# Kernel optimization log

Measured on AMD Instinct MI355X. Metric: run time of the kernel, lower is better.

## Reference

```python
import jax, jax.numpy as jnp
import numpy as np


def _ln(x, w, b):
    m = x.mean(-1, keepdims=True)
    v = x.var(-1, keepdims=True)
    return (x - m) * jax.lax.rsqrt(v + 1e-5) * w + b


def setup_inputs() -> dict:
    key = jax.random.key(0)
    ks = jax.random.split(key, 12)
    B, Cm, T, D, H = 8, 192, 2048, 512, 1536
    n_fft, hop = 1024, 256
    nF = n_fft // 2 + 1
    s = 0.05
    rn = lambda k, shape: jax.random.normal(k, shape, jnp.float32) * s
    window = (0.5 - 0.5 * jnp.cos(2.0 * jnp.pi * jnp.arange(n_fft, dtype=jnp.float32) / n_fft))
    return dict(
        mel=jax.random.normal(ks[0], (B, Cm, T), jnp.float32),
        embed_w=rn(ks[1], (D, Cm, 7)), embed_b=rn(ks[2], (D,)),
        norm_w=jnp.ones((D,), jnp.float32), norm_b=jnp.zeros((D,), jnp.float32),
        blk_dw_w=rn(ks[3], (8, D, 1, 7)), blk_dw_b=rn(ks[4], (8, D)),
        blk_norm_w=jnp.ones((8, D), jnp.float32), blk_norm_b=jnp.zeros((8, D), jnp.float32),
        blk_pw1_w=rn(ks[5], (8, H, D)), blk_pw1_b=rn(ks[6], (8, H)),
        blk_pw2_w=rn(ks[7], (8, D, H)), blk_pw2_b=rn(ks[8], (8, D)),
        blk_gamma=jnp.full((8, D), 0.1, jnp.float32),
        fnorm_w=jnp.ones((D,), jnp.float32), fnorm_b=jnp.zeros((D,), jnp.float32),
        head_w=rn(ks[9], (2 * nF, D)), head_b=rn(ks[10], (2 * nF,)),
        window=window,
        n_fft=n_fft, hop_length=hop,
    )


def _vocoder(mel, embed_w, embed_b, norm_w, norm_b,
             blk_dw_w, blk_dw_b, blk_norm_w, blk_norm_b,
             blk_pw1_w, blk_pw1_b, blk_pw2_w, blk_pw2_b, blk_gamma,
             fnorm_w, fnorm_b, head_w, head_b, window, n_fft, hop_length):
    D = embed_w.shape[0]
    # embed conv: [B,192,T] -> [B,512,T]
    x = jax.lax.conv_general_dilated(mel, embed_w, (1,), [(3, 3)],
                                     dimension_numbers=('NCH', 'OIH', 'NCH'))
    x = x + embed_b[None, :, None]
    x = _ln(x.transpose(0, 2, 1), norm_w, norm_b).transpose(0, 2, 1)

    def blk(x, p):
        dw, db, nw, nb, w1, b1, w2, b2, g = p
        y = jax.lax.conv_general_dilated(x, dw, (1,), [(3, 3)],
                                         dimension_numbers=('NCH', 'OIH', 'NCH'),
                                         feature_group_count=D)
        y = y + db[None, :, None]
        y = _ln(y.transpose(0, 2, 1), nw, nb)          # [B,T,D]
        y = jax.nn.gelu(jnp.einsum('btc,hc->bth', y, w1) + b1, approximate=False)
        y = jnp.einsum('bth,ch->btc', y, w2) + b2
        return x + (g * y).transpose(0, 2, 1), None

    x, _ = jax.lax.scan(blk, x, (blk_dw_w, blk_dw_b, blk_norm_w, blk_norm_b,
                                 blk_pw1_w, blk_pw1_b, blk_pw2_w, blk_pw2_b, blk_gamma))

    h = _ln(x.transpose(0, 2, 1), fnorm_w, fnorm_b)    # [B,T,D]
    out = jnp.einsum('btc,fc->btf', h, head_w) + head_b  # [B,T,2*nF]
    nF = n_fft // 2 + 1
    mag = jnp.minimum(jnp.exp(out[..., :nF]), 100.0)   # [B,T,nF]
    phase = out[..., nF:]
    S_real = mag * jnp.cos(phase)
    S_imag = mag * jnp.sin(phase)

    # real inverse-DFT basis
    n = jnp.arange(n_fft, dtype=jnp.float32)
    k = jnp.arange(nF, dtype=jnp.float32)
    ang = 2.0 * jnp.pi * n[:, None] * k[None, :] / n_fft
    scale = jnp.full((nF,), 2.0 / n_fft, jnp.float32)
    scale = scale.at[0].set(1.0 / n_fft)
    if n_fft % 2 == 0:
        scale = scale.at[-1].set(1.0 / n_fft)
    cos_b = jnp.cos(ang) * scale[None, :]              # [n_fft, nF]
    sin_b = jnp.sin(ang) * scale[None, :]

    frames = (jnp.einsum('btf,nf->btn', S_real, cos_b)
              - jnp.einsum('btf,nf->btn', S_imag, sin_b))  # [B,T,n_fft]
    frames = frames * window[None, None, :]

    B, T, N = frames.shape
    L = (T - 1) * hop_length + n_fft
    idx = jnp.arange(T)[:, None] * hop_length + jnp.arange(n_fft)[None, :]  # [T,n_fft]
    audio = jnp.zeros((B, L), frames.dtype).at[:, idx].add(frames)
    win_sq = window * window
    win_env = jnp.zeros((L,), frames.dtype).at[idx].add(
        jnp.broadcast_to(win_sq, (T, n_fft)))
    audio = audio / (win_env[None, :] + 1e-11)
    c = n_fft // 2
    return audio[:, c:-c]


def reference(mel, embed_w, embed_b, norm_w, norm_b,
              blk_dw_w, blk_dw_b, blk_norm_w, blk_norm_b,
              blk_pw1_w, blk_pw1_b, blk_pw2_w, blk_pw2_b, blk_gamma,
              fnorm_w, fnorm_b, head_w, head_b, window, n_fft, hop_length):
    return _vocoder(mel, embed_w, embed_b, norm_w, norm_b,
                    blk_dw_w, blk_dw_b, blk_norm_w, blk_norm_b,
                    blk_pw1_w, blk_pw1_b, blk_pw2_w, blk_pw2_b, blk_gamma,
                    fnorm_w, fnorm_b, head_w, head_b, window, n_fft, hop_length)
```

## Files before the change

kernel.cpp:

```cpp
#include <hip/hip_runtime.h>
#include <cmath>

#define B_ 8
#define T_ 2048
#define BT_ 16384
#define D_ 512
#define H_ 1536
#define CM_ 192
#define KE_ 1344
#define TP_ 2054
#define NFFT_ 1024
#define NF_ 513
#define HOP_ 256
#define NO2_ 1026
#define NPAD_ 1152
#define KI_ 1088
#define LOUT_ 524032

typedef _Float16 f16;
typedef f16 f16x8 __attribute__((ext_vector_type(8)));
typedef float f32x4 __attribute__((ext_vector_type(4)));

__device__ __forceinline__ float gelu_f(float v) {
    float u = 0.7978845608028654f * v * (1.0f + 0.044715f * v * v);
    float e = __expf(2.0f * u);
    float t = 1.0f - 2.0f * __builtin_amdgcn_rcpf(e + 1.0f);
    return 0.5f * v * (1.0f + t);
}

__device__ __forceinline__ void gload16(const void* g, void* s) {
    __builtin_amdgcn_global_load_lds((const __attribute__((address_space(1))) void*)g,
                                     (__attribute__((address_space(3))) void*)s, 16, 0, 0);
}

__global__ __launch_bounds__(256) void k_prep(const float* __restrict__ bw1,
                                              const float* __restrict__ bw2,
                                              const float* __restrict__ embed_w,
                                              const float* __restrict__ hw,
                                              const float* __restrict__ hb,
                                              const float* __restrict__ bdw,
                                              f16* __restrict__ w1_h,
                                              f16* __restrict__ w2_h,
                                              f16* __restrict__ we_h,
                                              f16* __restrict__ head_h,
                                              float* __restrict__ hb_pad,
                                              float* __restrict__ dwT,
                                              f16* __restrict__ wmat_h) {
    int i = blockIdx.x * 256 + threadIdx.x;
    if (i < 6291456) { w1_h[i] = (f16)bw1[i]; return; }
    i -= 6291456;
    if (i < 6291456) { w2_h[i] = (f16)bw2[i]; return; }
    i -= 6291456;
    if (i < 688128) {
        int d = i / KE_;
        int r2 = i - d * KE_;
        int tap = r2 / CM_;
        int c = r2 - tap * CM_;
        we_h[i] = (f16)embed_w[(d * CM_ + c) * 7 + tap];
        return;
    }
    i -= 688128;
    if (i < 589824) {
        int row = i >> 9;
        head_h[i] = (row < NO2_) ? (f16)hw[i] : (f16)0.0f;
        return;
    }
    i -= 589824;
    if (i < 1152) { hb_pad[i] = (i < NO2_) ? hb[i] : 0.0f; return; }
    i -= 1152;
    if (i < 28672) {
        int bl = i / 3584;
        int rem = i - bl * 3584;
        int k = rem >> 9;
        int d = rem & 511;
        dwT[i] = bdw[bl * 3584 + d * 7 + k];
        return;
    }
    i -= 28672;
    if (i < 1114112) {
        int n = i / KI_;
        int f2 = i - n * KI_;
        float v = 0.0f;
        if (f2 < NF_) {
            int r = (n * f2) & (NFFT_ - 1);
            float sc = (f2 == 0 || f2 == NF_ - 1) ? (1.0f / NFFT_) : (2.0f / NFFT_);
            v = cospif((float)r * (2.0f / NFFT_)) * sc;
        } else if (f2 < NO2_) {
            int f = f2 - NF_;
            int r = (n * f) & (NFFT_ - 1);
            float sc = (f == 0 || f == NF_ - 1) ? (1.0f / NFFT_) : (2.0f / NFFT_);
            v = -sinpif((float)r * (2.0f / NFFT_)) * sc;
        }
        wmat_h[i] = (f16)v;
    }
}

__global__ __launch_bounds__(256) void k_melT(const float* __restrict__ mel,
                                              f16* __restrict__ mt) {
    int idx = blockIdx.x * 256 + threadIdx.x;
    if (idx >= B_ * TP_ * 24) return;
    int c8 = idx % 24;
    int rem = idx / 24;
    int tp = rem % TP_;
    int b = rem / TP_;
    int t = tp - 3;
    f16x8 v;
    if (t >= 0 && t < T_) {
        const float* mp = mel + ((size_t)b * CM_ + c8 * 8) * T_ + t;
#pragma unroll
        for (int i = 0; i < 8; ++i) v[i] = (f16)mp[(size_t)i * T_];
    } else {
#pragma unroll
        for (int i = 0; i < 8; ++i) v[i] = (f16)0.0f;
    }
    *(f16x8*)(mt + (size_t)idx * 8) = v;
}

__global__ __launch_bounds__(64) void k_lnh(const f16* __restrict__ in,
                                            f16* __restrict__ out,
                                            const float* __restrict__ w,
                                            const float* __restrict__ b) {
    int row = blockIdx.x;
    int lane = threadIdx.x;
    f16x8 hv = *(const f16x8*)(in + (size_t)row * D_ + lane * 8);
    float x[8];
#pragma unroll
    for (int i = 0; i < 8; ++i) x[i] = (float)hv[i];
    float s = 0.f, ss = 0.f;
#pragma unroll
    for (int i = 0; i < 8; ++i) { s += x[i]; ss = fmaf(x[i], x[i], ss); }
#pragma unroll
    for (int off = 32; off > 0; off >>= 1) {
        s  += __shfl_xor(s, off);
        ss += __shfl_xor(ss, off);
    }
    float mean = s * (1.0f / 512.0f);
    float var  = ss * (1.0f / 512.0f) - mean * mean;
    float rs = rsqrtf(var + 1e-5f);
    const float* wp = w + lane * 8;
    const float* bp = b + lane * 8;
    float4 w0 = *(const float4*)wp, w1 = *(const float4*)(wp + 4);
    float4 b0 = *(const float4*)bp, b1 = *(const float4*)(bp + 4);
    float wv[8] = {w0.x, w0.y, w0.z, w0.w, w1.x, w1.y, w1.z, w1.w};
    float bv[8] = {b0.x, b0.y, b0.z, b0.w, b1.x, b1.y, b1.z, b1.w};
    f16x8 h;
#pragma unroll
    for (int i = 0; i < 8; ++i) h[i] = (f16)((x[i] - mean) * rs * wv[i] + bv[i]);
    *(f16x8*)(out + (size_t)row * D_ + lane * 8) = h;
}

__global__ __launch_bounds__(256) void k_dwln2h(const f16* __restrict__ x,
                                                const float* __restrict__ dwT,
                                                const float* __restrict__ db,
                                                const float* __restrict__ nw,
                                                const float* __restrict__ nb,
                                                f16* __restrict__ out) {
    __shared__ float xs[22][512];
    int tid = threadIdx.x;
    int blk = blockIdx.x;
    int b = blk >> 7;
    int t0 = (blk & 127) << 4;
    const f16* xb = x + ((size_t)b << 20);
#pragma unroll
    for (int i = 0; i < 6; ++i) {
        int idx = tid + (i << 8);
        if (idx < 22 * 64) {
            int row = idx >> 6;
            int c8 = idx & 63;
            int t = t0 + row - 3;
            float v[8];
            if (t >= 0 && t < T_) {
                f16x8 hv = *(const f16x8*)(xb + ((size_t)t << 9) + (c8 << 3));
#pragma unroll
                for (int u = 0; u < 8; ++u) v[u] = (float)hv[u];
            } else {
#pragma unroll
                for (int u = 0; u < 8; ++u) v[u] = 0.0f;
            }
            *(float4*)&xs[row][c8 << 3] = make_float4(v[0], v[1], v[2], v[3]);
            *(float4*)&xs[row][(c8 << 3) + 4] = make_float4(v[4], v[5], v[6], v[7]);
        }
    }
    __syncthreads();

    int o = tid & 63;
    int slot = tid >> 6;
    int d0 = o << 3;
    float acc[4][8];
    {
        float4 b0 = *(const float4*)(db + d0);
        float4 b1 = *(const float4*)(db + d0 + 4);
#pragma unroll
        for (int u = 0; u < 4; ++u) {
            acc[u][0] = b0.x; acc[u][1] = b0.y; acc[u][2] = b0.z; acc[u][3] = b0.w;
            acc[u][4] = b1.x; acc[u][5] = b1.y; acc[u][6] = b1.z; acc[u][7] = b1.w;
        }
    }
#pragma unroll
    for (int k = 0; k < 7; ++k) {
        float w8[8];
        *(float4*)&w8[0] = *(const float4*)(dwT + (k << 9) + d0);
        *(float4*)&w8[4] = *(const float4*)(dwT + (k << 9) + d0 + 4);
#pragma unroll
        for (int u = 0; u < 4; ++u) {
            int row = (slot << 2) + u + k;
            float x8[8];
            *(float4*)&x8[0] = *(const float4*)&xs[row][d0];
            *(float4*)&x8[4] = *(const float4*)&xs[row][d0 + 4];
#pragma unroll
            for (int i = 0; i < 8; ++i) acc[u][i] = fmaf(w8[i], x8[i], acc[u][i]);
        }
    }
    float4 w0 = *(const float4*)(nw + d0), w1 = *(const float4*)(nw + d0 + 4);
    float4 n0 = *(const float4*)(nb + d0), n1 = *(const float4*)(nb + d0 + 4);
    float nwv[8] = {w0.x, w0.y, w0.z, w0.w, w1.x, w1.y, w1.z, w1.w};
    float nbv[8] = {n0.x, n0.y, n0.z, n0.w, n1.x, n1.y, n1.z, n1.w};
#pragma unroll
    for (int u = 0; u < 4; ++u) {
        float s = 0.f, ss = 0.f;
#pragma unroll
        for (int i = 0; i < 8; ++i) { s += acc[u][i]; ss = fmaf(acc[u][i], acc[u][i], ss); }
#pragma unroll
        for (int off = 32; off > 0; off >>= 1) {
            s  += __shfl_xor(s, off);
            ss += __shfl_xor(ss, off);
        }
        float mean = s * (1.0f / 512.0f);
        float var  = ss * (1.0f / 512.0f) - mean * mean;
        float rs = rsqrtf(var + 1e-5f);
        f16x8 h;
#pragma unroll
        for (int i = 0; i < 8; ++i)
            h[i] = (f16)((acc[u][i] - mean) * rs * nwv[i] + nbv[i]);
        int t = t0 + (slot << 2) + u;
        *(f16x8*)(out + (((size_t)(b << 11) + t) << 9) + d0) = h;
    }
}

#define MF(d, a, b) d = __builtin_amdgcn_mfma_f32_16x16x32_f16(a, b, d, 0, 0, 0)

#define TSZ_ 4096

__device__ __forceinline__ void stage32(const f16* __restrict__ g, f16* s,
                                        int lda, int kof, int tid) {
    int dr0 = tid >> 3;
    int sl  = tid & 7;
#pragma unroll
    for (int i = 0; i < 2; ++i) {
        int d  = dr0 + (i << 5);
        int gs = sl ^ (d & 7);
        int row = (d << 1) + (gs >> 2);
        int kc  = gs & 3;
        gload16(g + (size_t)row * lda + kof + (kc << 3),
                s + (d << 6) + (sl << 3));
    }
}

template <int EPI, bool EMBED>
__global__ __launch_bounds__(256, 3) void k_hgemm5(const f16* __restrict__ A,
                                                   const f16* __restrict__ W,
                                                   const float* __restrict__ bias,
                                                   const float* __restrict__ gamma,
                                                   void* __restrict__ C,
                                                   int K, int ldc, int nNt) {
    __shared__ f16 lds[3 * 2 * TSZ_];
    int tid = threadIdx.x;
    int nwg = gridDim.x, bid = blockIdx.x;
    int q = nwg >> 3, r = nwg & 7;
    int xcd = bid & 7, lin = bid >> 3;
    int swz = (xcd < r ? xcd * (q + 1) : r * (q + 1) + (xcd - r) * q) + lin;
    int bm = (swz / nNt) << 7;
    int bn = (swz % nNt) << 7;
    const f16* gA;
    int lda;
    if constexpr (EMBED) {
        gA = A + ((size_t)((bm >> 11) * TP_) + (bm & (T_ - 1))) * CM_;
        lda = CM_;
    } else {
        gA = A + (size_t)bm * K;
        lda = K;
    }
    const f16* gW = W + (size_t)bn * K;

    int l = tid & 63;
    int wv = tid >> 6;
    int wm = (wv & 1) << 6;
    int wn = (wv >> 1) << 6;
    int lr = l & 15;
    int lk = l >> 4;
    int lrh = lr >> 1;
    int s0l = ((lr & 1) << 2) | lk;

    int offA[4], offB[4];
#pragma unroll
    for (int i = 0; i < 4; ++i) {
        int dA = (wm >> 1) + i * 8 + lrh;
        offA[i] = (dA << 6) + ((s0l ^ (dA & 7)) << 3);
        int dB = (wn >> 1) + i * 8 + lrh;
        offB[i] = (dB << 6) + ((s0l ^ (dB & 7)) << 3);
    }

    f32x4 acc[4][4];
#pragma unroll
    for (int i = 0; i < 4; ++i)
#pragma unroll
        for (int j = 0; j < 4; ++j) acc[i][j] = {0.f, 0.f, 0.f, 0.f};

    int nk = K >> 5;
    f16* s0 = lds;
    f16* s1 = lds + 2 * TSZ_;
    f16* s2 = lds + 4 * TSZ_;

    stage32(gA, s0, lda, 0, tid);      stage32(gW, s0 + TSZ_, K, 0, tid);
    stage32(gA, s1, lda, 32, tid);     stage32(gW, s1 + TSZ_, K, 32, tid);
    asm volatile("s_waitcnt vmcnt(4)" ::: "memory");
    __builtin_amdgcn_s_barrier();

    for (int t = 0; t < nk; ++t) {
        bool stg = (t + 2 < nk);
        if (stg) {
            int ko = (t + 2) << 5;
            stage32(gA, s2, lda, ko, tid);
            stage32(gW, s2 + TSZ_, K, ko, tid);
        }
        f16x8 af[4], bf[4];
#pragma unroll
        for (int i = 0; i < 4; ++i) af[i] = *(const f16x8*)(s0 + offA[i]);
#pragma unroll
        for (int j = 0; j < 4; ++j) bf[j] = *(const f16x8*)(s0 + TSZ_ + offB[j]);
        __builtin_amdgcn_s_setprio(1);
#pragma unroll
        for (int i = 0; i < 4; ++i)
#pragma unroll
            for (int j = 0; j < 4; ++j) MF(acc[i][j], af[i], bf[j]);
        __builtin_amdgcn_s_setprio(0);
        if (stg)               asm volatile("s_waitcnt vmcnt(4)" ::: "memory");
        else if (t + 1 < nk)   asm volatile("s_waitcnt vmcnt(0)" ::: "memory");
        if (t + 1 < nk) {
            __builtin_amdgcn_s_barrier();
            asm volatile("" ::: "memory");
        }
        f16* tmp = s0; s0 = s1; s1 = s2; s2 = tmp;
    }

    int lk4 = lk << 2;
#pragma unroll
    for (int i = 0; i < 4; ++i) {
#pragma unroll
        for (int rr = 0; rr < 4; ++rr) {
            int row = bm + wm + i * 16 + lk4 + rr;
            size_t moff = (size_t)row * ldc;
#pragma unroll
            for (int j = 0; j < 4; ++j) {
                int col = bn + wn + j * 16 + lr;
                float v = acc[i][j][rr];
                if constexpr (EPI == 0) {
                    ((float*)C)[moff + col] = v + bias[col];
                } else if constexpr (EPI == 1) {
                    ((f16*)C)[moff + col] = (f16)gelu_f(v + bias[col]);
                } else if constexpr (EPI == 4) {
                    ((f16*)C)[moff + col] = (f16)(v + bias[col]);
                } else if constexpr (EPI == 5) {
                    f16* Cp = (f16*)C;
                    float old = (float)Cp[moff + col];
                    Cp[moff + col] = (f16)(old + gamma[col] * (v + bias[col]));
                } else {
                    ((f16*)C)[moff + col] = (f16)(v * bias[col]);
                }
            }
        }
    }
}

#define ASZ_ 8192
#define RSZ_ 12288

__device__ __forceinline__ void stageA256(const f16* __restrict__ g, f16* s,
                                          int K, int kof, int tid) {
    int dr0 = tid >> 3;
    int sl  = tid & 7;
#pragma unroll
    for (int i = 0; i < 4; ++i) {
        int d  = dr0 + (i << 5);
        int gs = sl ^ (d & 7);
        int row = (d << 1) + (gs >> 2);
        int kc  = gs & 3;
        gload16(g + (size_t)row * K + kof + (kc << 3),
                s + (d << 6) + (sl << 3));
    }
}

__device__ __forceinline__ void stageB128(const f16* __restrict__ g, f16* s,
                                          int K, int kof, int tid) {
    int dr0 = tid >> 3;
    int sl  = tid & 7;
#pragma unroll
    for (int i = 0; i < 2; ++i) {
        int d  = dr0 + (i << 5);
        int gs = sl ^ (d & 7);
        int row = (d << 1) + (gs >> 2);
        int kc  = gs & 3;
        gload16(g + (size_t)row * K + kof + (kc << 3),
                s + (d << 6) + (sl << 3));
    }
}

template <int EPI>
__global__ __launch_bounds__(256, 2) void k_hgemm7(const f16* __restrict__ A,
                                                   const f16* __restrict__ W,
                                                   const float* __restrict__ bias,
                                                   const float* __restrict__ gamma,
                                                   void* __restrict__ C,
                                                   int K, int ldc, int nNt) {
    __shared__ f16 lds[3 * RSZ_];
    int tid = threadIdx.x;
    int nwg = gridDim.x, bid = blockIdx.x;
    int q = nwg >> 3, r = nwg & 7;
    int xcd = bid & 7, lin = bid >> 3;
    int swz = (xcd < r ? xcd * (q + 1) : r * (q + 1) + (xcd - r) * q) + lin;
    int bm = (swz / nNt) << 8;
    int bn = (swz % nNt) << 7;
    const f16* gA = A + (size_t)bm * K;
    const f16* gW = W + (size_t)bn * K;

    int l = tid & 63;
    int wv = tid >> 6;
    int wm = (wv & 1) << 7;
    int wn = (wv >> 1) << 6;
    int lr = l & 15;
    int lk = l >> 4;
    int lrh = lr >> 1;
    int s0l = ((lr & 1) << 2) | lk;

    int offA[8], offB[4];
#pragma unroll
    for (int i = 0; i < 8; ++i) {
        int dA = (wm >> 1) + i * 8 + lrh;
        offA[i] = (dA << 6) + ((s0l ^ (dA & 7)) << 3);
    }
#pragma unroll
    for (int j = 0; j < 4; ++j) {
        int dB = (wn >> 1) + j * 8 + lrh;
        offB[j] = (dB << 6) + ((s0l ^ (dB & 7)) << 3);
    }

    f32x4 acc[8][4];
#pragma unroll
    for (int i = 0; i < 8; ++i)
#pragma unroll
        for (int j = 0; j < 4; ++j) acc[i][j] = {0.f, 0.f, 0.f, 0.f};

    int nk = K >> 5;
    f16* s0 = lds;
    f16* s1 = lds + RSZ_;
    f16* s2 = lds + 2 * RSZ_;

    stageA256(gA, s0, K, 0, tid);      stageB128(gW, s0 + ASZ_, K, 0, tid);
    stageA256(gA, s1, K, 32, tid);     stageB128(gW, s1 + ASZ_, K, 32, tid);
    asm volatile("s_waitcnt vmcnt(6)" ::: "memory");
    __builtin_amdgcn_s_barrier();

    for (int t = 0; t < nk; ++t) {
        bool stg = (t + 2 < nk);
        if (stg) {
            int ko = (t + 2) << 5;
            stageA256(gA, s2, K, ko, tid);
            stageB128(gW, s2 + ASZ_, K, ko, tid);
        }
        f16x8 af[8], bf[4];
#pragma unroll
        for (int i = 0; i < 8; ++i) af[i] = *(const f16x8*)(s0 + offA[i]);
#pragma unroll
        for (int j = 0; j < 4; ++j) bf[j] = *(const f16x8*)(s0 + ASZ_ + offB[j]);
        __builtin_amdgcn_s_setprio(1);
#pragma unroll
        for (int i = 0; i < 8; ++i)
#pragma unroll
            for (int j = 0; j < 4; ++j) MF(acc[i][j], af[i], bf[j]);
        __builtin_amdgcn_s_setprio(0);
        if (stg)               asm volatile("s_waitcnt vmcnt(6)" ::: "memory");
        else if (t + 1 < nk)   asm volatile("s_waitcnt vmcnt(0)" ::: "memory");
        if (t + 1 < nk) {
            __builtin_amdgcn_s_barrier();
            asm volatile("" ::: "memory");
        }
        f16* tmp = s0; s0 = s1; s1 = s2; s2 = tmp;
    }

    int lk4 = lk << 2;
#pragma unroll
    for (int i = 0; i < 8; ++i) {
#pragma unroll
        for (int rr = 0; rr < 4; ++rr) {
            int row = bm + wm + i * 16 + lk4 + rr;
            size_t moff = (size_t)row * ldc;
#pragma unroll
            for (int j = 0; j < 4; ++j) {
                int col = bn + wn + j * 16 + lr;
                float v = acc[i][j][rr];
                if constexpr (EPI == 0) {
                    ((float*)C)[moff + col] = v + bias[col];
                } else {
                    ((f16*)C)[moff + col] = (f16)(v * bias[col]);
                }
            }
        }
    }
}

__global__ __launch_bounds__(256) void k_srsi(const float* __restrict__ o,
                                              f16* __restrict__ S) {
    int idx = blockIdx.x * 256 + threadIdx.x;
    if (idx >= BT_ * KI_) return;
    int m = idx / KI_;
    int f2 = idx - m * KI_;
    size_t base = (size_t)m * NPAD_;
    float v = 0.0f;
    if (f2 < NF_) {
        float mag = fminf(__expf(o[base + f2]), 100.0f);
        float sn, cs;
        __sincosf(o[base + NF_ + f2], &sn, &cs);
        v = mag * cs;
    } else if (f2 < NO2_) {
        int f = f2 - NF_;
        float mag = fminf(__expf(o[base + f]), 100.0f);
        float sn, cs;
        __sincosf(o[base + NF_ + f], &sn, &cs);
        v = mag * sn;
    }
    S[idx] = (f16)v;
}

__global__ __launch_bounds__(256) void k_gather(const f16* __restrict__ frames,
                                                const float* __restrict__ win,
                                                float* __restrict__ out) {
    int idx = blockIdx.x * 256 + threadIdx.x;
    int b  = idx / LOUT_;
    int lp = idx - b * LOUT_;
    int l = lp + (NFFT_ / 2);
    int thi = l >> 8;
    if (thi > T_ - 1) thi = T_ - 1;
    int tlo = l - (NFFT_ - 1) + (HOP_ - 1);
    tlo = (tlo < 0) ? 0 : (tlo >> 8);
    float num = 0.0f, den = 0.0f;
    for (int t = tlo; t <= thi; ++t) {
        int n = l - (t << 8);
        float wv = win[n];
        num += (float)frames[((size_t)(b * T_ + t) << 10) + n];
        den = fmaf(wv, wv, den);
    }
    out[idx] = num / (den + 1e-11f);
}

extern "C" void kernel_launch(void* const* d_in, const int* in_sizes, int n_in,
                              void* d_out, int out_size, void* d_ws, size_t ws_size,
                              hipStream_t stream) {
    (void)in_sizes; (void)n_in; (void)out_size; (void)ws_size;
    const float* mel     = (const float*)d_in[0];
    const float* embed_w = (const float*)d_in[1];
    const float* embed_b = (const float*)d_in[2];
    const float* norm_w  = (const float*)d_in[3];
    const float* norm_b  = (const float*)d_in[4];
    const float* bdw = (const float*)d_in[5];
    const float* bdb = (const float*)d_in[6];
    const float* bnw = (const float*)d_in[7];
    const float* bnb = (const float*)d_in[8];
    const float* bw1 = (const float*)d_in[9];
    const float* bb1 = (const float*)d_in[10];
    const float* bw2 = (const float*)d_in[11];
    const float* bb2 = (const float*)d_in[12];
    const float* bg  = (const float*)d_in[13];
    const float* fnw = (const float*)d_in[14];
    const float* fnb = (const float*)d_in[15];
    const float* hw  = (const float*)d_in[16];
    const float* hb  = (const float*)d_in[17];
    const float* win = (const float*)d_in[18];

    char* ws = (char*)d_ws;
    f16*   xbuf_h = (f16*)ws;
    f16*   ybuf_h = (f16*)(ws + 33554432);
    f16*   S_h    = (f16*)ws;
    char* R = ws + 50331648;
    f16*   melTp  = (f16*)R;
    f16*   hbuf_h = (f16*)(R + 33554432);
    float* obuf   = (float*)R;
    f16*   frames_h = (f16*)R;
    char* Wr = ws + 134217728;
    f16*   w1_h   = (f16*)Wr;
    f16*   w2_h   = (f16*)(Wr + 12582912);
    f16*   head_h = (f16*)(Wr + 25165824);
    f16*   wmat_h = (f16*)(Wr + 26345472);
    f16*   we_h   = (f16*)(Wr + 28573696);
    float* hb_pad = (float*)(Wr + 29949952);
    float* dwT    = (float*)(Wr + 29954560);

    k_prep<<<58613, 256, 0, stream>>>(bw1, bw2, embed_w, hw, hb, bdw,
                                      w1_h, w2_h, we_h, head_h, hb_pad, dwT, wmat_h);
    k_melT<<<(B_ * TP_ * 24 + 255) / 256, 256, 0, stream>>>(mel, melTp);

    k_hgemm5<4, true><<<128 * 4, 256, 0, stream>>>(melTp, we_h, embed_b, nullptr, xbuf_h,
                                                   KE_, D_, 4);
    k_lnh<<<BT_, 64, 0, stream>>>(xbuf_h, xbuf_h, norm_w, norm_b);

    for (int bl = 0; bl < 8; ++bl) {
        k_dwln2h<<<B_ * 128, 256, 0, stream>>>(xbuf_h, dwT + bl * 3584, bdb + bl * D_,
                                               bnw + bl * D_, bnb + bl * D_, ybuf_h);
        k_hgemm5<1, false><<<128 * 12, 256, 0, stream>>>(ybuf_h, w1_h + (size_t)bl * H_ * D_,
                                                         bb1 + bl * H_, nullptr, hbuf_h,
                                                         D_, H_, 12);
        k_hgemm5<5, false><<<128 * 4, 256, 0, stream>>>(hbuf_h, w2_h + (size_t)bl * D_ * H_,
                                                        bb2 + bl * D_, bg + bl * D_, xbuf_h,
                                                        H_, D_, 4);
    }

    k_lnh<<<BT_, 64, 0, stream>>>(xbuf_h, ybuf_h, fnw, fnb);
    k_hgemm5<0, false><<<128 * 9, 256, 0, stream>>>(ybuf_h, head_h, hb_pad, nullptr, obuf,
                                                    D_, NPAD_, 9);
    k_srsi<<<(BT_ * KI_ + 255) / 256, 256, 0, stream>>>(obuf, S_h);
    k_hgemm7<3><<<64 * 8, 256, 0, stream>>>(S_h, wmat_h, win, nullptr, frames_h,
                                            KI_, NFFT_, 8);
    k_gather<<<B_ * LOUT_ / 256, 256, 0, stream>>>(frames_h, win, (float*)d_out);
}
```

Baseline: 965.0 us.

## Fuse magnitude/phase-to-spectrum into head GEMM epilogue and merge mel transpose into prep

The head weight and bias rows are interleaved so that each magnitude/phase pair lands on neighbouring lanes. The GEMM epilogue then swaps partners with a shuffle, computes exp, clamps, takes sincos and writes the f16 real/imag spectrum straight into S. This removes the fp32 head output buffer and the separate k_srsi pass over it. The mel transpose kernel is also folded into the prep kernel to save a launch. Padding columns of S past 1026 are no longer zeroed and now hold whatever was left in the aliased buffer, relying on the zero rows of the inverse-DFT matrix.

```diff
diff --git a/kernel.cpp b/kernel.cpp
--- a/kernel.cpp
+++ b/kernel.cpp
@@ -39,13 +39,15 @@
                                               const float* __restrict__ hw,
                                               const float* __restrict__ hb,
                                               const float* __restrict__ bdw,
+                                              const float* __restrict__ mel,
                                               f16* __restrict__ w1_h,
                                               f16* __restrict__ w2_h,
                                               f16* __restrict__ we_h,
                                               f16* __restrict__ head_h,
                                               float* __restrict__ hb_pad,
                                               float* __restrict__ dwT,
-                                              f16* __restrict__ wmat_h) {
+                                              f16* __restrict__ wmat_h,
+                                              f16* __restrict__ melTp) {
     int i = blockIdx.x * 256 + threadIdx.x;
     if (i < 6291456) { w1_h[i] = (f16)bw1[i]; return; }
     i -= 6291456;
@@ -62,11 +64,25 @@
     i -= 688128;
     if (i < 589824) {
         int row = i >> 9;
-        head_h[i] = (row < NO2_) ? (f16)hw[i] : (f16)0.0f;
+        int k = i & 511;
+        f16 v = (f16)0.0f;
+        if (row < NO2_) {
+            int src = (row & 1) ? (NF_ + (row >> 1)) : (row >> 1);
+            v = (f16)hw[(size_t)src * D_ + k];
+        }
+        head_h[i] = v;
         return;
     }
     i -= 589824;
-    if (i < 1152) { hb_pad[i] = (i < NO2_) ? hb[i] : 0.0f; return; }
+    if (i < 1152) {
+        float v = 0.0f;
+        if (i < NO2_) {
+            int src = (i & 1) ? (NF_ + (i >> 1)) : (i >> 1);
+            v = hb[src];
+        }
+        hb_pad[i] = v;
+        return;
+    }
     i -= 1152;
     if (i < 28672) {
         int bl = i / 3584;
@@ -92,28 +108,26 @@
             v = -sinpif((float)r * (2.0f / NFFT_)) * sc;
         }
         wmat_h[i] = (f16)v;
-    }
-}
-
-__global__ __launch_bounds__(256) void k_melT(const float* __restrict__ mel,
-                                              f16* __restrict__ mt) {
-    int idx = blockIdx.x * 256 + threadIdx.x;
-    if (idx >= B_ * TP_ * 24) return;
-    int c8 = idx % 24;
-    int rem = idx / 24;
-    int tp = rem % TP_;
-    int b = rem / TP_;
-    int t = tp - 3;
-    f16x8 v;
-    if (t >= 0 && t < T_) {
-        const float* mp = mel + ((size_t)b * CM_ + c8 * 8) * T_ + t;
-#pragma unroll
-        for (int i = 0; i < 8; ++i) v[i] = (f16)mp[(size_t)i * T_];
-    } else {
-#pragma unroll
-        for (int i = 0; i < 8; ++i) v[i] = (f16)0.0f;
-    }
-    *(f16x8*)(mt + (size_t)idx * 8) = v;
+        return;
+    }
+    i -= 1114112;
+    if (i < B_ * TP_ * 24) {
+        int c8 = i % 24;
+        int rem = i / 24;
+        int tp = rem % TP_;
+        int b = rem / TP_;
+        int t = tp - 3;
+        f16x8 v;
+        if (t >= 0 && t < T_) {
+            const float* mp = mel + ((size_t)b * CM_ + c8 * 8) * T_ + t;
+#pragma unroll
+            for (int u = 0; u < 8; ++u) v[u] = (f16)mp[(size_t)u * T_];
+        } else {
+#pragma unroll
+            for (int u = 0; u < 8; ++u) v[u] = (f16)0.0f;
+        }
+        *(f16x8*)(melTp + (size_t)i * 8) = v;
+    }
 }
 
 __global__ __launch_bounds__(64) void k_lnh(const f16* __restrict__ in,
@@ -354,9 +368,7 @@
             for (int j = 0; j < 4; ++j) {
                 int col = bn + wn + j * 16 + lr;
                 float v = acc[i][j][rr];
-                if constexpr (EPI == 0) {
-                    ((float*)C)[moff + col] = v + bias[col];
-                } else if constexpr (EPI == 1) {
+                if constexpr (EPI == 1) {
                     ((f16*)C)[moff + col] = (f16)gelu_f(v + bias[col]);
                 } else if constexpr (EPI == 4) {
                     ((f16*)C)[moff + col] = (f16)(v + bias[col]);
@@ -364,6 +376,19 @@
                     f16* Cp = (f16*)C;
                     float old = (float)Cp[moff + col];
                     Cp[moff + col] = (f16)(old + gamma[col] * (v + bias[col]));
+                } else if constexpr (EPI == 6) {
+                    float vb = v + bias[col];
+                    float w2 = __shfl_xor(vb, 1);
+                    float a = (lr & 1) ? w2 : vb;
+                    float bph = (lr & 1) ? vb : w2;
+                    float mag = fminf(__expf(a), 100.0f);
+                    float sn, cs;
+                    __sincosf(bph, &sn, &cs);
+                    float sval = (lr & 1) ? mag * sn : mag * cs;
+                    int f = col >> 1;
+                    int dst = (lr & 1) ? (NF_ + f) : f;
+                    if (col < NO2_)
+                        ((f16*)C)[moff + dst] = (f16)sval;
                 } else {
                     ((f16*)C)[moff + col] = (f16)(v * bias[col]);
                 }
@@ -506,29 +531,6 @@
             }
         }
     }
-}
-
-__global__ __launch_bounds__(256) void k_srsi(const float* __restrict__ o,
-                                              f16* __restrict__ S) {
-    int idx = blockIdx.x * 256 + threadIdx.x;
-    if (idx >= BT_ * KI_) return;
-    int m = idx / KI_;
-    int f2 = idx - m * KI_;
-    size_t base = (size_t)m * NPAD_;
-    float v = 0.0f;
-    if (f2 < NF_) {
-        float mag = fminf(__expf(o[base + f2]), 100.0f);
-        float sn, cs;
-        __sincosf(o[base + NF_ + f2], &sn, &cs);
-        v = mag * cs;
-    } else if (f2 < NO2_) {
-        int f = f2 - NF_;
-        float mag = fminf(__expf(o[base + f]), 100.0f);
-        float sn, cs;
-        __sincosf(o[base + NF_ + f], &sn, &cs);
-        v = mag * sn;
-    }
-    S[idx] = (f16)v;
 }
 
 __global__ __launch_bounds__(256) void k_gather(const f16* __restrict__ frames,
@@ -583,7 +585,6 @@
     char* R = ws + 50331648;
     f16*   melTp  = (f16*)R;
     f16*   hbuf_h = (f16*)(R + 33554432);
-    float* obuf   = (float*)R;
     f16*   frames_h = (f16*)R;
     char* Wr = ws + 134217728;
     f16*   w1_h   = (f16*)Wr;
@@ -594,9 +595,9 @@
     float* hb_pad = (float*)(Wr + 29949952);
     float* dwT    = (float*)(Wr + 29954560);
 
-    k_prep<<<58613, 256, 0, stream>>>(bw1, bw2, embed_w, hw, hb, bdw,
-                                      w1_h, w2_h, we_h, head_h, hb_pad, dwT, wmat_h);
-    k_melT<<<(B_ * TP_ * 24 + 255) / 256, 256, 0, stream>>>(mel, melTp);
+    k_prep<<<60153, 256, 0, stream>>>(bw1, bw2, embed_w, hw, hb, bdw, mel,
+                                      w1_h, w2_h, we_h, head_h, hb_pad, dwT,
+                                      wmat_h, melTp);
 
     k_hgemm5<4, true><<<128 * 4, 256, 0, stream>>>(melTp, we_h, embed_b, nullptr, xbuf_h,
                                                    KE_, D_, 4);
@@ -614,9 +615,8 @@
     }
 
     k_lnh<<<BT_, 64, 0, stream>>>(xbuf_h, ybuf_h, fnw, fnb);
-    k_hgemm5<0, false><<<128 * 9, 256, 0, stream>>>(ybuf_h, head_h, hb_pad, nullptr, obuf,
-                                                    D_, NPAD_, 9);
-    k_srsi<<<(BT_ * KI_ + 255) / 256, 256, 0, stream>>>(obuf, S_h);
+    k_hgemm5<6, false><<<128 * 9, 256, 0, stream>>>(ybuf_h, head_h, hb_pad, nullptr, S_h,
+                                                    D_, KI_, 9);
     k_hgemm7<3><<<64 * 8, 256, 0, stream>>>(S_h, wmat_h, win, nullptr, frames_h,
                                             KI_, NFFT_, 8);
     k_gather<<<B_ * LOUT_ / 256, 256, 0, stream>>>(frames_h, win, (float*)d_out);
```

Measured after the change: 942.0 us. 1.02x faster.
